# Kernel optimization log

Hardware: AMD Instinct MI355X
Metric: run time of the kernel (lower is better)

## Reference

```python
import math
import jax, jax.numpy as jnp
import numpy as np

B, S, HID, NH = 8, 512, 1024, 16
D = HID // NH          # head dim = 64
SPAN = 512             # att_span = max_relative_positions = max_position_embeddings


def _linear(x, W, b):
    # torch nn.Linear: y = x @ W.T + b, W is [out, in]
    return jnp.einsum('...i,oi->...o', x, W) + b


def _heads(x):
    # [B, S, HID] -> [B, NH, S, D]
    b, s, _ = x.shape
    return x.reshape(b, s, NH, D).transpose(0, 2, 1, 3)


def setup_inputs() -> dict:
    key = jax.random.key(0)
    ks = jax.random.split(key, 16)
    f = lambda i, shape, sc=1.0: jax.random.normal(ks[i], shape, dtype=jnp.float32) * sc
    return {
        'q': f(0, (B, S, HID)),
        'k': f(1, (B, S, HID)),
        'v': f(2, (B, S, HID)),
        'attention_mask': jnp.tril(jnp.ones((S, S), dtype=bool))[None, None],  # causal [1,1,S,S]
        'Wq': f(3, (HID, HID), 0.02), 'bq': jnp.zeros((HID,), jnp.float32),
        'Wk': f(4, (HID, HID), 0.02), 'bk': jnp.zeros((HID,), jnp.float32),
        'Wv': f(5, (HID, HID), 0.02), 'bv': jnp.zeros((HID,), jnp.float32),
        'Wpk': f(6, (HID, HID), 0.02), 'bpk': jnp.zeros((HID,), jnp.float32),
        'Wpq': f(7, (HID, HID), 0.02), 'bpq': jnp.zeros((HID,), jnp.float32),
        'rel_emb': f(8, (2 * SPAN, HID), 0.02),
    }


def reference(q, k, v, attention_mask, Wq, bq, Wk, bk, Wv, bv, Wpk, bpk, Wpq, bpq, rel_emb):
    scale_factor = 3  # 1 (content) + c2p + p2c
    scale = 1.0 / math.sqrt(D * scale_factor)

    ql = _heads(_linear(q, Wq, bq))   # [B,NH,S,D]
    kl = _heads(_linear(k, Wk, bk))
    vl = _heads(_linear(v, Wv, bv))

    # content-to-content scores
    scores = jnp.einsum('bhqd,bhkd->bhqk', ql, kl) * scale

    # relative positions (no bucketing since position_buckets = -1)
    rel = jnp.arange(S)[:, None] - jnp.arange(S)[None, :]          # [S,S]
    c2p_pos = jnp.clip(rel + SPAN, 0, 2 * SPAN - 1)
    p2c_pos = jnp.clip(-rel + SPAN, 0, 2 * SPAN - 1)

    # projected relative-position embeddings -> [NH, 2*SPAN, D]
    pk = _linear(rel_emb, Wpk, bpk).reshape(2 * SPAN, NH, D).transpose(1, 0, 2)
    pq = _linear(rel_emb, Wpq, bpq).reshape(2 * SPAN, NH, D).transpose(1, 0, 2)

    # content-to-position: out[b,h,q,k] = (q . pos_key)[b,h,q, c2p_pos[q,k]]
    c2p = jnp.einsum('bhqd,hjd->bhqj', ql, pk) * scale             # [B,NH,S,2*SPAN]
    c2p = jnp.take_along_axis(c2p, jnp.broadcast_to(c2p_pos[None, None], (B, NH, S, S)), axis=-1)

    # position-to-content: gathered[b,h,k,q] = (k . pos_query)[b,h,k, p2c_pos[k,q]], then transpose
    p2c = jnp.einsum('bhkd,hjd->bhkj', kl, pq) * scale             # [B,NH,S,2*SPAN]
    p2c = jnp.take_along_axis(p2c, jnp.broadcast_to(p2c_pos[None, None], (B, NH, S, S)), axis=-1)

    scores = scores + c2p + jnp.swapaxes(p2c, -1, -2)
    # subtract detached row max (as in torch: .max(...).values.detach())
    scores = scores - jax.lax.stop_gradient(scores.max(axis=-1, keepdims=True))

    # XSoftmax: masked softmax, then zero masked positions
    neg = jnp.float32(-1e30)
    probs = jax.nn.softmax(jnp.where(attention_mask, scores, neg), axis=-1)
    probs = jnp.where(attention_mask, probs, 0.0)

    ctx = jnp.einsum('bhqk,bhkd->bhqd', probs, vl)                 # [B,NH,S,D]
    return ctx.transpose(0, 2, 1, 3).reshape(B, S, HID)
```

## Files before the change

kernel.cpp:

```cpp
#include <hip/hip_runtime.h>
#include <hip/hip_bf16.h>
#include <math.h>

#define SCALE 0.07216878364870323f
#define NEG_BIG -1e30f

typedef __attribute__((ext_vector_type(8))) short bf16x8;
typedef __attribute__((ext_vector_type(4))) short bf16x4;
typedef __attribute__((ext_vector_type(4))) float f32x4;
#define MFMA_BF16 __builtin_amdgcn_mfma_f32_16x16x32_bf16

static __device__ __forceinline__ float bf2f(__hip_bfloat16 x) { return __bfloat162float(x); }
static __device__ __forceinline__ __hip_bfloat16 f2bf(float x) { return __float2bfloat16(x); }
static __device__ __forceinline__ short f2bs(float x) {
  union { __hip_bfloat16 b; short s; } u; u.b = __float2bfloat16(x); return u.s;
}
static __device__ __forceinline__ float s2f(short v) {
  union { float f; unsigned u; } x; x.u = ((unsigned)(unsigned short)v) << 16; return x.f;
}
static __device__ __forceinline__ bf16x4 cvt4(float4 f) {
  bf16x4 r; r[0] = f2bs(f.x); r[1] = f2bs(f.y); r[2] = f2bs(f.z); r[3] = f2bs(f.w);
  return r;
}
static __device__ __forceinline__ bf16x8 ldg8(const __hip_bfloat16* p) {
  return *(const bf16x8*)p;
}
static __device__ __forceinline__ void gl_lds16(const __hip_bfloat16* g, __hip_bfloat16* l) {
  __builtin_amdgcn_global_load_lds(
      (const __attribute__((address_space(1))) void*)g,
      (__attribute__((address_space(3))) void*)l, 16, 0, 0);
}

struct CvtJob { const float* src; __hip_bfloat16* dst; int n4; };
struct CvtArgs { CvtJob j[9]; };

__global__ __launch_bounds__(256) void cvt_kernel(CvtArgs a) {
  const CvtJob jb = a.j[blockIdx.y];
  const float4* s = (const float4*)jb.src;
  bf16x4* d = (bf16x4*)jb.dst;
  const int stride = gridDim.x * 256;
  for (int i = blockIdx.x * 256 + threadIdx.x; i < jb.n4; i += stride)
    d[i] = cvt4(s[i]);
}

struct Gemm { const __hip_bfloat16* A; const __hip_bfloat16* W;
              const float* bias; __hip_bfloat16* out; int mode; int mBits; int nBlk;
              float oscale; };
struct ProjArgs { Gemm g[5]; };

static __device__ __forceinline__ void stage_tile(const __hip_bfloat16* gtile,
                                                  __hip_bfloat16* ltile,
                                                  int nrows, int wave, int lane) {
  const int r = lane >> 3;
  const int chunk = (lane & 7) ^ r;
#pragma unroll
  for (int c = 0; c < 4; c++) {
    if (c * 64 >= nrows) break;
    const int rowbase = c * 64 + wave * 8;
    gl_lds16(gtile + (size_t)(rowbase + r) * 1024 + chunk * 8,
             ltile + (size_t)rowbase * 64);
  }
}

__global__ __launch_bounds__(512, 2) void proj_kernel(ProjArgs pa) {
  const Gemm g = pa.g[blockIdx.y];
  if ((int)blockIdx.x >= g.nBlk) return;
  __shared__ __hip_bfloat16 As[256][64];
  __shared__ __hip_bfloat16 Ws[128][64];

  const int bid = blockIdx.x;
  const int m0 = (bid & ((1 << g.mBits) - 1)) * 256;
  const int n0 = (bid >> g.mBits) * 128;
  const int tid = threadIdx.x;
  const int wave = tid >> 6, lane = tid & 63;
  const int q16 = lane >> 4, l16 = lane & 15;
  const int wr = wave >> 1, wc = wave & 1;
  const int l7 = l16 & 7;

  const __hip_bfloat16* Ag = g.A + (size_t)m0 * 1024;
  const __hip_bfloat16* Wg = g.W + (size_t)n0 * 1024;

  f32x4 acc[4][4] = {};

  for (int t = 0; t < 16; ++t) {
    __syncthreads();
    stage_tile(Ag + t * 64, &As[0][0], 256, wave, lane);
    stage_tile(Wg + t * 64, &Ws[0][0], 128, wave, lane);
    __syncthreads();
#pragma unroll
    for (int kh = 0; kh < 2; kh++) {
      const int csw = ((kh * 4 + q16) ^ l7) * 8;
      bf16x8 bw[4], af[4];
#pragma unroll
      for (int ni = 0; ni < 4; ni++)
        bw[ni] = *(const bf16x8*)(&Ws[wc * 64 + ni * 16 + l16][0] + csw);
#pragma unroll
      for (int mi = 0; mi < 4; mi++)
        af[mi] = *(const bf16x8*)(&As[wr * 64 + mi * 16 + l16][0] + csw);
      __builtin_amdgcn_s_setprio(1);
#pragma unroll
      for (int ni = 0; ni < 4; ni++)
#pragma unroll
        for (int mi = 0; mi < 4; mi++)
          acc[mi][ni] = MFMA_BF16(af[mi], bw[ni], acc[mi][ni], 0, 0, 0);
      __builtin_amdgcn_s_setprio(0);
    }
  }

#pragma unroll
  for (int ni = 0; ni < 4; ni++) {
    const int n = n0 + wc * 64 + ni * 16 + l16;
#pragma unroll
    for (int mi = 0; mi < 4; mi++) {
#pragma unroll
      for (int rr = 0; rr < 4; rr++) {
        const int m = m0 + wr * 64 + mi * 16 + q16 * 4 + rr;
        float val = acc[mi][ni][rr];
        size_t oidx;
        if (g.mode == 0) {
          val = (val + g.bias[n]) * g.oscale;
          const int b = m >> 9, s = m & 511;
          const int h = n >> 6, d = n & 63;
          oidx = ((size_t)((b * 16 + h) * 512 + s)) * 64 + d;
        } else if (g.mode == 1) {
          val = (val + g.bias[m]) * g.oscale;
          const int b = n >> 9, s = n & 511;
          const int h = m >> 6, d = m & 63;
          oidx = ((size_t)((b * 16 + h) * 64 + d)) * 512 + s;
        } else {
          val = (val + g.bias[n]) * g.oscale;
          const int h = n >> 6, d = n & 63;
          oidx = ((size_t)(h * 512 + m)) * 64 + d;
        }
        g.out[oidx] = f2bf(val);
      }
    }
  }
}

__global__ __launch_bounds__(256) void attn_kernel(
    const __hip_bfloat16* __restrict__ ql,
    const __hip_bfloat16* __restrict__ kl,
    const __hip_bfloat16* __restrict__ vlT,
    const __hip_bfloat16* __restrict__ pk,
    const __hip_bfloat16* __restrict__ pq,
    float* __restrict__ out)
{
  __shared__ __align__(16) __hip_bfloat16 pool[2][64][72];
  __shared__ __align__(16) __hip_bfloat16 pqs[2][32][72];
  __shared__ __align__(16) float qkbuf[32][36];
  __shared__ __align__(16) __hip_bfloat16 cpb[2][32][68];
  __shared__ __align__(16) __hip_bfloat16 pT[64][36];
  __shared__ __align__(16) __hip_bfloat16 ptile[32][40];
  __shared__ __align__(16) __hip_bfloat16 vt[64][40];
  __shared__ float mred[32];
  __shared__ float rsum[32];

  const int bid = blockIdx.x;
  const int qt = 15 - (bid >> 7);
  const int bh = bid & 127;
  const int h = bh & 15, b = bh >> 4;
  const int q0 = qt * 32;

  const __hip_bfloat16* qlp = ql + (size_t)bh * 512 * 64;
  const __hip_bfloat16* klp = kl + (size_t)bh * 512 * 64;
  const __hip_bfloat16* vtp = vlT + (size_t)bh * 64 * 512;
  const __hip_bfloat16* pkp = pk + (size_t)h * 512 * 64;
  const __hip_bfloat16* pqp = pq + (size_t)h * 512 * 64;

  const int tid = threadIdx.x, wave = tid >> 6, lane = tid & 63;
  const int q16 = lane >> 4, l16 = lane & 15;
  const int wr = wave & 1, wc = wave >> 1;

  bf16x8 qlB[2][2];
#pragma unroll
  for (int ksi = 0; ksi < 2; ksi++)
#pragma unroll
    for (int bq = 0; bq < 2; bq++)
      qlB[ksi][bq] = ldg8(qlp + (size_t)(q0 + bq * 16 + l16) * 64 + ksi * 32 + q16 * 8);

  {
    int4 z = {0, 0, 0, 0};
    *(int4*)(&pqs[1][tid >> 3][(tid & 7) * 8]) = z;
  }

  const int kEnd = q0 + 32;
  const int nIter = kEnd >> 5;

  const int sr = tid >> 3, sseg = tid & 7;
  const int vr = tid >> 2, vs = tid & 3;
  int4 rKv, rPKv, rPQv, rVt;
  {
    rKv  = ((const int4*)(klp + (size_t)(q0 + sr) * 64))[sseg];
    rPKv = ((const int4*)(pkp + (size_t)(0 + sr) * 64))[sseg];
    rPQv = ((const int4*)(pqp + (size_t)(0 + sr) * 64))[sseg];
    rVt  = ((const int4*)(vtp + (size_t)vr * 512 + q0))[vs];
  }

  const int aq = tid >> 3;
  const int kb = (tid & 7) * 4;
  float m_old = -INFINITY, s_part = 0.f;
  f32x4 octx[2] = {};

  for (int it = 0; it < nIter; ++it) {
    const int k0 = q0 - it * 32;
    const int par = it & 1;
    *(int4*)(&pool[par][sr][sseg * 8])      = rKv;
    *(int4*)(&pool[par][32 + sr][sseg * 8]) = rPKv;
    *(int4*)(&pqs[par][sr][sseg * 8])       = rPQv;
    if (it + 1 < nIter) {
      const int k0n = k0 - 32, jbn = (it + 1) * 32;
      rKv  = ((const int4*)(klp + (size_t)(k0n + sr) * 64))[sseg];
      rPKv = ((const int4*)(pkp + (size_t)(jbn + sr) * 64))[sseg];
      rPQv = ((const int4*)(pqp + (size_t)(jbn + sr) * 64))[sseg];
    }
    __syncthreads();

    const int arb = (wave == 1) ? 32 : 0;
    f32x4 a4[2][2] = {};
    __builtin_amdgcn_s_setprio(1);
#pragma unroll
    for (int ksi = 0; ksi < 2; ksi++) {
      const int ko = ksi * 32 + q16 * 8;
      bf16x8 Af0 = *(const bf16x8*)(&pool[par][arb + l16][ko]);
      bf16x8 Af1 = *(const bf16x8*)(&pool[par][arb + 16 + l16][ko]);
      bf16x8 Bf0, Bf1;
      if (wave < 2) {
        Bf0 = qlB[ksi][0];
        Bf1 = qlB[ksi][1];
      } else {
        const int ps = (wave == 2) ? (par ^ 1) : par;
        Bf0 = *(const bf16x8*)(&pqs[ps][l16][ko]);
        Bf1 = *(const bf16x8*)(&pqs[ps][16 + l16][ko]);
      }
      a4[0][0] = MFMA_BF16(Af0, Bf0, a4[0][0], 0, 0, 0);
      a4[0][1] = MFMA_BF16(Af0, Bf1, a4[0][1], 0, 0, 0);
      a4[1][0] = MFMA_BF16(Af1, Bf0, a4[1][0], 0, 0, 0);
      a4[1][1] = MFMA_BF16(Af1, Bf1, a4[1][1], 0, 0, 0);
    }
    __builtin_amdgcn_s_setprio(0);
    if (wave == 0) {
#pragma unroll
      for (int a = 0; a < 2; a++)
#pragma unroll
        for (int bq = 0; bq < 2; bq++)
          *(f32x4*)(&qkbuf[bq * 16 + l16][a * 16 + q16 * 4]) = a4[a][bq];
    } else if (wave == 1) {
#pragma unroll
      for (int a = 0; a < 2; a++)
#pragma unroll
        for (int bq = 0; bq < 2; bq++) {
          bf16x4 v;
#pragma unroll
          for (int r = 0; r < 4; r++) v[r] = f2bs(a4[a][bq][r]);
          const int q = bq * 16 + l16, jr = a * 16 + q16 * 4;
          *(bf16x4*)(&cpb[par][q][32 + jr]) = v;
          *(bf16x4*)(&cpb[par ^ 1][q][jr]) = v;
        }
    } else {
      const int rb = (wave == 3) ? 32 : 0;
#pragma unroll
      for (int a = 0; a < 2; a++)
#pragma unroll
        for (int bq = 0; bq < 2; bq++) {
          bf16x4 v;
#pragma unroll
          for (int r = 0; r < 4; r++) v[r] = f2bs(a4[a][bq][r]);
          *(bf16x4*)(&pT[rb + bq * 16 + l16][a * 16 + q16 * 4]) = v;
        }
    }
    __syncthreads();

    {
      const f32x4 qk4 = *(const f32x4*)(&qkbuf[aq][kb]);
      float v[4];
      float tmax = -INFINITY;
#pragma unroll
      for (int j = 0; j < 4; j++) {
        const int dlt = aq - (kb + j);
        v[j] = qk4[j] + bf2f(cpb[par][aq][dlt + 32]) + bf2f(pT[dlt + 32][kb + j]);
        if ((it == 0) && (dlt < 0)) v[j] = -INFINITY;
        else tmax = fmaxf(tmax, v[j]);
      }
      tmax = fmaxf(tmax, __shfl_xor(tmax, 1));
      tmax = fmaxf(tmax, __shfl_xor(tmax, 2));
      tmax = fmaxf(tmax, __shfl_xor(tmax, 4));
      const float m_new = fmaxf(m_old, tmax);
      const float f = __expf(m_old - m_new);
      bf16x4 pv4;
      float psum = 0.f;
#pragma unroll
      for (int j = 0; j < 4; j++) {
        const float p = __expf(v[j] - m_new);
        pv4[j] = f2bs(p);
        psum += p;
      }
      s_part = s_part * f + psum;
      m_old = m_new;
      *(bf16x4*)(&ptile[aq][kb]) = pv4;
      if ((tid & 7) == 0) mred[aq] = f;
    }
    {
      *(int4*)(&vt[vr][vs * 8]) = rVt;
      if (it + 1 < nIter)
        rVt = ((const int4*)(vtp + (size_t)vr * 512 + (k0 - 32)))[vs];
    }
    __syncthreads();

    {
      float fr[4];
#pragma unroll
      for (int rr = 0; rr < 4; rr++) fr[rr] = mred[wr * 16 + q16 * 4 + rr];
      bf16x8 af = *(const bf16x8*)(&ptile[wr * 16 + l16][q16 * 8]);
      __builtin_amdgcn_s_setprio(1);
#pragma unroll
      for (int cs = 0; cs < 2; cs++) {
        bf16x8 bv = *(const bf16x8*)(&vt[wc * 32 + cs * 16 + l16][q16 * 8]);
        f32x4 c = octx[cs];
#pragma unroll
        for (int rr = 0; rr < 4; rr++) c[rr] *= fr[rr];
        octx[cs] = MFMA_BF16(af, bv, c, 0, 0, 0);
      }
      __builtin_amdgcn_s_setprio(0);
    }
  }

  {
    float s = s_part;
    s += __shfl_xor(s, 1);
    s += __shfl_xor(s, 2);
    s += __shfl_xor(s, 4);
    if ((tid & 7) == 0) rsum[aq] = s;
  }
  __syncthreads();

  for (int cs = 0; cs < 2; cs++) {
    const int d = wc * 32 + cs * 16 + l16;
    for (int rr = 0; rr < 4; rr++) {
      const int qh = wr * 16 + q16 * 4 + rr;
      const float val = octx[cs][rr] / rsum[qh];
      out[((size_t)(b * 512 + q0 + qh)) * 1024 + h * 64 + d] = val;
    }
  }
}

extern "C" void kernel_launch(void* const* d_in, const int* in_sizes, int n_in,
                              void* d_out, int out_size, void* d_ws, size_t ws_size,
                              hipStream_t stream) {
  const float* q   = (const float*)d_in[0];
  const float* k   = (const float*)d_in[1];
  const float* v   = (const float*)d_in[2];
  const float* Wq  = (const float*)d_in[4];
  const float* bq  = (const float*)d_in[5];
  const float* Wk  = (const float*)d_in[6];
  const float* bk  = (const float*)d_in[7];
  const float* Wv  = (const float*)d_in[8];
  const float* bv  = (const float*)d_in[9];
  const float* Wpk = (const float*)d_in[10];
  const float* bpk = (const float*)d_in[11];
  const float* Wpq = (const float*)d_in[12];
  const float* bpq = (const float*)d_in[13];
  const float* rel = (const float*)d_in[14];
  float* out = (float*)d_out;

  char* ws = (char*)d_ws;
  const size_t MB = 1u << 20;
  __hip_bfloat16* bqi  = (__hip_bfloat16*)(ws);
  __hip_bfloat16* bki  = (__hip_bfloat16*)(ws + 8 * MB);
  __hip_bfloat16* bvi  = (__hip_bfloat16*)(ws + 16 * MB);
  __hip_bfloat16* bWq  = (__hip_bfloat16*)(ws + 24 * MB);
  __hip_bfloat16* bWk  = (__hip_bfloat16*)(ws + 26 * MB);
  __hip_bfloat16* bWv  = (__hip_bfloat16*)(ws + 28 * MB);
  __hip_bfloat16* bWpk = (__hip_bfloat16*)(ws + 30 * MB);
  __hip_bfloat16* bWpq = (__hip_bfloat16*)(ws + 32 * MB);
  __hip_bfloat16* brel = (__hip_bfloat16*)(ws + 34 * MB);
  __hip_bfloat16* wql  = (__hip_bfloat16*)(ws + 35 * MB);
  __hip_bfloat16* wkl  = (__hip_bfloat16*)(ws + 43 * MB);
  __hip_bfloat16* wvlT = (__hip_bfloat16*)(ws + 51 * MB);
  __hip_bfloat16* wpk  = (__hip_bfloat16*)(ws + 59 * MB);
  __hip_bfloat16* wpq  = (__hip_bfloat16*)(ws + 60 * MB);

  CvtArgs ca;
  ca.j[0] = { q,   bqi,  4194304 / 4 };
  ca.j[1] = { k,   bki,  4194304 / 4 };
  ca.j[2] = { v,   bvi,  4194304 / 4 };
  ca.j[3] = { Wq,  bWq,  1048576 / 4 };
  ca.j[4] = { Wk,  bWk,  1048576 / 4 };
  ca.j[5] = { Wv,  bWv,  1048576 / 4 };
  ca.j[6] = { Wpk, bWpk, 1048576 / 4 };
  ca.j[7] = { Wpq, bWpq, 1048576 / 4 };
  ca.j[8] = { rel + (size_t)512 * 1024, brel, 524288 / 4 };
  cvt_kernel<<<dim3(1024, 9), 256, 0, stream>>>(ca);

  ProjArgs pj;
  pj.g[0] = { bqi,  bWq,  bq,  wql,  0, 4, 128, SCALE };
  pj.g[1] = { bki,  bWk,  bk,  wkl,  0, 4, 128, 1.0f };
  pj.g[2] = { bWv,  bvi,  bv,  wvlT, 1, 2, 128, 1.0f };
  pj.g[3] = { brel, bWpk, bpk, wpk,  2, 1, 16,  1.0f };
  pj.g[4] = { brel, bWpq, bpq, wpq,  2, 1, 16,  SCALE };
  proj_kernel<<<dim3(128, 5), 512, 0, stream>>>(pj);

  attn_kernel<<<2048, 256, 0, stream>>>(wql, wkl, wvlT, wpk, wpq, out);
}
```

Before: 222.8 us.

## Software-pipeline attention loop and pre-gather relative-position bias tiles

Restructures the attention loop so the PV MFMA for the previous tile runs at the top of the next iteration, and the K/PK/PQ shared-memory stores for the next tile are merged into an earlier phase. This removes one __syncthreads per iteration. The c2p and p2c results are now scattered directly into diagonal-gathered layouts (cpexp, pTexp), so the softmax phase reads contiguous 4-wide vectors instead of doing strided scalar gathers. The cost is scalar, conditional scatter stores with possible bank conflicts during the write phase, plus a prologue and an epilogue.

```diff
diff --git a/kernel.cpp b/kernel.cpp
--- a/kernel.cpp
+++ b/kernel.cpp
@@ -149,8 +149,8 @@
   __shared__ __align__(16) __hip_bfloat16 pool[2][64][72];
   __shared__ __align__(16) __hip_bfloat16 pqs[2][32][72];
   __shared__ __align__(16) float qkbuf[32][36];
-  __shared__ __align__(16) __hip_bfloat16 cpb[2][32][68];
-  __shared__ __align__(16) __hip_bfloat16 pT[64][36];
+  __shared__ __align__(16) __hip_bfloat16 cpexp[2][32][36];
+  __shared__ __align__(16) __hip_bfloat16 pTexp[32][36];
   __shared__ __align__(16) __hip_bfloat16 ptile[32][40];
   __shared__ __align__(16) __hip_bfloat16 vt[64][40];
   __shared__ float mred[32];
@@ -178,11 +178,6 @@
 #pragma unroll
     for (int bq = 0; bq < 2; bq++)
       qlB[ksi][bq] = ldg8(qlp + (size_t)(q0 + bq * 16 + l16) * 64 + ksi * 32 + q16 * 8);
-
-  {
-    int4 z = {0, 0, 0, 0};
-    *(int4*)(&pqs[1][tid >> 3][(tid & 7) * 8]) = z;
-  }
 
   const int kEnd = q0 + 32;
   const int nIter = kEnd >> 5;
@@ -197,6 +192,20 @@
     rVt  = ((const int4*)(vtp + (size_t)vr * 512 + q0))[vs];
   }
 
+  {
+    int4 z = {0, 0, 0, 0};
+    *(int4*)(&pqs[1][sr][sseg * 8]) = z;
+    *(int4*)(&pool[0][sr][sseg * 8])      = rKv;
+    *(int4*)(&pool[0][32 + sr][sseg * 8]) = rPKv;
+    *(int4*)(&pqs[0][sr][sseg * 8])       = rPQv;
+    if (1 < nIter) {
+      rKv  = ((const int4*)(klp + (size_t)(q0 - 32 + sr) * 64))[sseg];
+      rPKv = ((const int4*)(pkp + (size_t)(32 + sr) * 64))[sseg];
+      rPQv = ((const int4*)(pqp + (size_t)(32 + sr) * 64))[sseg];
+    }
+  }
+  __syncthreads();
+
   const int aq = tid >> 3;
   const int kb = (tid & 7) * 4;
   float m_old = -INFINITY, s_part = 0.f;
@@ -205,81 +214,95 @@
   for (int it = 0; it < nIter; ++it) {
     const int k0 = q0 - it * 32;
     const int par = it & 1;
-    *(int4*)(&pool[par][sr][sseg * 8])      = rKv;
-    *(int4*)(&pool[par][32 + sr][sseg * 8]) = rPKv;
-    *(int4*)(&pqs[par][sr][sseg * 8])       = rPQv;
-    if (it + 1 < nIter) {
-      const int k0n = k0 - 32, jbn = (it + 1) * 32;
-      rKv  = ((const int4*)(klp + (size_t)(k0n + sr) * 64))[sseg];
-      rPKv = ((const int4*)(pkp + (size_t)(jbn + sr) * 64))[sseg];
-      rPQv = ((const int4*)(pqp + (size_t)(jbn + sr) * 64))[sseg];
-    }
-    __syncthreads();
-
-    const int arb = (wave == 1) ? 32 : 0;
-    f32x4 a4[2][2] = {};
-    __builtin_amdgcn_s_setprio(1);
-#pragma unroll
-    for (int ksi = 0; ksi < 2; ksi++) {
-      const int ko = ksi * 32 + q16 * 8;
-      bf16x8 Af0 = *(const bf16x8*)(&pool[par][arb + l16][ko]);
-      bf16x8 Af1 = *(const bf16x8*)(&pool[par][arb + 16 + l16][ko]);
-      bf16x8 Bf0, Bf1;
-      if (wave < 2) {
-        Bf0 = qlB[ksi][0];
-        Bf1 = qlB[ksi][1];
+
+    if (it > 0) {
+      float fr[4];
+#pragma unroll
+      for (int rr = 0; rr < 4; rr++) fr[rr] = mred[wr * 16 + q16 * 4 + rr];
+      bf16x8 af = *(const bf16x8*)(&ptile[wr * 16 + l16][q16 * 8]);
+#pragma unroll
+      for (int cs = 0; cs < 2; cs++) {
+        bf16x8 bv = *(const bf16x8*)(&vt[wc * 32 + cs * 16 + l16][q16 * 8]);
+        f32x4 c = octx[cs];
+#pragma unroll
+        for (int rr = 0; rr < 4; rr++) c[rr] *= fr[rr];
+        octx[cs] = MFMA_BF16(af, bv, c, 0, 0, 0);
+      }
+    }
+    {
+      const int arb = (wave == 1) ? 32 : 0;
+      f32x4 a4[2][2] = {};
+      __builtin_amdgcn_s_setprio(1);
+#pragma unroll
+      for (int ksi = 0; ksi < 2; ksi++) {
+        const int ko = ksi * 32 + q16 * 8;
+        bf16x8 Af0 = *(const bf16x8*)(&pool[par][arb + l16][ko]);
+        bf16x8 Af1 = *(const bf16x8*)(&pool[par][arb + 16 + l16][ko]);
+        bf16x8 Bf0, Bf1;
+        if (wave < 2) {
+          Bf0 = qlB[ksi][0];
+          Bf1 = qlB[ksi][1];
+        } else {
+          const int ps = (wave == 2) ? (par ^ 1) : par;
+          Bf0 = *(const bf16x8*)(&pqs[ps][l16][ko]);
+          Bf1 = *(const bf16x8*)(&pqs[ps][16 + l16][ko]);
+        }
+        a4[0][0] = MFMA_BF16(Af0, Bf0, a4[0][0], 0, 0, 0);
+        a4[0][1] = MFMA_BF16(Af0, Bf1, a4[0][1], 0, 0, 0);
+        a4[1][0] = MFMA_BF16(Af1, Bf0, a4[1][0], 0, 0, 0);
+        a4[1][1] = MFMA_BF16(Af1, Bf1, a4[1][1], 0, 0, 0);
+      }
+      __builtin_amdgcn_s_setprio(0);
+      if (wave == 0) {
+#pragma unroll
+        for (int a = 0; a < 2; a++)
+#pragma unroll
+          for (int bq = 0; bq < 2; bq++)
+            *(f32x4*)(&qkbuf[bq * 16 + l16][a * 16 + q16 * 4]) = a4[a][bq];
+      } else if (wave == 1) {
+#pragma unroll
+        for (int a = 0; a < 2; a++)
+#pragma unroll
+          for (int bq = 0; bq < 2; bq++) {
+            const int q = bq * 16 + l16;
+#pragma unroll
+            for (int r = 0; r < 4; r++) {
+              const int jr = a * 16 + q16 * 4 + r;
+              const short val = f2bs(a4[a][bq][r]);
+              if (jr <= q) ((short*)&cpexp[par][q][0])[q - jr] = val;
+              else         ((short*)&cpexp[par ^ 1][q][0])[q + 32 - jr] = val;
+            }
+          }
       } else {
-        const int ps = (wave == 2) ? (par ^ 1) : par;
-        Bf0 = *(const bf16x8*)(&pqs[ps][l16][ko]);
-        Bf1 = *(const bf16x8*)(&pqs[ps][16 + l16][ko]);
-      }
-      a4[0][0] = MFMA_BF16(Af0, Bf0, a4[0][0], 0, 0, 0);
-      a4[0][1] = MFMA_BF16(Af0, Bf1, a4[0][1], 0, 0, 0);
-      a4[1][0] = MFMA_BF16(Af1, Bf0, a4[1][0], 0, 0, 0);
-      a4[1][1] = MFMA_BF16(Af1, Bf1, a4[1][1], 0, 0, 0);
-    }
-    __builtin_amdgcn_s_setprio(0);
-    if (wave == 0) {
-#pragma unroll
-      for (int a = 0; a < 2; a++)
-#pragma unroll
-        for (int bq = 0; bq < 2; bq++)
-          *(f32x4*)(&qkbuf[bq * 16 + l16][a * 16 + q16 * 4]) = a4[a][bq];
-    } else if (wave == 1) {
-#pragma unroll
-      for (int a = 0; a < 2; a++)
-#pragma unroll
-        for (int bq = 0; bq < 2; bq++) {
-          bf16x4 v;
-#pragma unroll
-          for (int r = 0; r < 4; r++) v[r] = f2bs(a4[a][bq][r]);
-          const int q = bq * 16 + l16, jr = a * 16 + q16 * 4;
-          *(bf16x4*)(&cpb[par][q][32 + jr]) = v;
-          *(bf16x4*)(&cpb[par ^ 1][q][jr]) = v;
-        }
-    } else {
-      const int rb = (wave == 3) ? 32 : 0;
-#pragma unroll
-      for (int a = 0; a < 2; a++)
-#pragma unroll
-        for (int bq = 0; bq < 2; bq++) {
-          bf16x4 v;
-#pragma unroll
-          for (int r = 0; r < 4; r++) v[r] = f2bs(a4[a][bq][r]);
-          *(bf16x4*)(&pT[rb + bq * 16 + l16][a * 16 + q16 * 4]) = v;
-        }
+        const int jjb = (wave == 3) ? 32 : 0;
+#pragma unroll
+        for (int a = 0; a < 2; a++)
+#pragma unroll
+          for (int bq = 0; bq < 2; bq++) {
+            const int jj = jjb + bq * 16 + l16;
+#pragma unroll
+            for (int r = 0; r < 4; r++) {
+              const int k = a * 16 + q16 * 4 + r;
+              const int q = k + jj - 32;
+              if (q >= 0 && q < 32)
+                ((short*)&pTexp[q][0])[k] = f2bs(a4[a][bq][r]);
+            }
+          }
+      }
     }
     __syncthreads();
 
     {
       const f32x4 qk4 = *(const f32x4*)(&qkbuf[aq][kb]);
+      const bf16x4 cp4 = *(const bf16x4*)(&cpexp[par][aq][kb]);
+      const bf16x4 p4  = *(const bf16x4*)(&pTexp[aq][kb]);
       float v[4];
       float tmax = -INFINITY;
 #pragma unroll
       for (int j = 0; j < 4; j++) {
-        const int dlt = aq - (kb + j);
-        v[j] = qk4[j] + bf2f(cpb[par][aq][dlt + 32]) + bf2f(pT[dlt + 32][kb + j]);
-        if ((it == 0) && (dlt < 0)) v[j] = -INFINITY;
+        v[j] = qk4[j] + s2f(cp4[j]) + s2f(p4[j]);
+        const bool msk = (it == 0) && (aq < kb + j);
+        if (msk) v[j] = -INFINITY;
         else tmax = fmaxf(tmax, v[j]);
       }
       tmax = fmaxf(tmax, __shfl_xor(tmax, 1));
@@ -305,23 +328,32 @@
       if (it + 1 < nIter)
         rVt = ((const int4*)(vtp + (size_t)vr * 512 + (k0 - 32)))[vs];
     }
+    if (it + 1 < nIter) {
+      *(int4*)(&pool[par ^ 1][sr][sseg * 8])      = rKv;
+      *(int4*)(&pool[par ^ 1][32 + sr][sseg * 8]) = rPKv;
+      *(int4*)(&pqs[par ^ 1][sr][sseg * 8])       = rPQv;
+      if (it + 2 < nIter) {
+        const int k02 = q0 - (it + 2) * 32, jb2 = (it + 2) * 32;
+        rKv  = ((const int4*)(klp + (size_t)(k02 + sr) * 64))[sseg];
+        rPKv = ((const int4*)(pkp + (size_t)(jb2 + sr) * 64))[sseg];
+        rPQv = ((const int4*)(pqp + (size_t)(jb2 + sr) * 64))[sseg];
+      }
+    }
     __syncthreads();
-
-    {
-      float fr[4];
-#pragma unroll
-      for (int rr = 0; rr < 4; rr++) fr[rr] = mred[wr * 16 + q16 * 4 + rr];
-      bf16x8 af = *(const bf16x8*)(&ptile[wr * 16 + l16][q16 * 8]);
-      __builtin_amdgcn_s_setprio(1);
-#pragma unroll
-      for (int cs = 0; cs < 2; cs++) {
-        bf16x8 bv = *(const bf16x8*)(&vt[wc * 32 + cs * 16 + l16][q16 * 8]);
-        f32x4 c = octx[cs];
-#pragma unroll
-        for (int rr = 0; rr < 4; rr++) c[rr] *= fr[rr];
-        octx[cs] = MFMA_BF16(af, bv, c, 0, 0, 0);
-      }
-      __builtin_amdgcn_s_setprio(0);
+  }
+
+  {
+    float fr[4];
+#pragma unroll
+    for (int rr = 0; rr < 4; rr++) fr[rr] = mred[wr * 16 + q16 * 4 + rr];
+    bf16x8 af = *(const bf16x8*)(&ptile[wr * 16 + l16][q16 * 8]);
+#pragma unroll
+    for (int cs = 0; cs < 2; cs++) {
+      bf16x8 bv = *(const bf16x8*)(&vt[wc * 32 + cs * 16 + l16][q16 * 8]);
+      f32x4 c = octx[cs];
+#pragma unroll
+      for (int rr = 0; rr < 4; rr++) c[rr] *= fr[rr];
+      octx[cs] = MFMA_BF16(af, bv, c, 0, 0, 0);
     }
   }
 
```

After: 217.5 us. 2.4% less time.
